# Kernel optimization log

Hardware: AMD Instinct MI355X
Metric: run time of the kernel (lower is better)

## Reference

```python
import jax, jax.numpy as jnp
import numpy as np

B = 65536          # bs * m
N_NODES = 2        # fixed by module usage (job-machine pair graphs)
IN_FEAT = 256
N_HEADS = 4
N_HIDDEN = 256     # concat=False -> n_hidden = out_features
SLOPE = 0.2


def setup_inputs() -> dict:
    key = jax.random.key(0)
    k_h, k_adj, k_w, k_a = jax.random.split(key, 4)
    h = jax.random.normal(k_h, (B, N_NODES, IN_FEAT), dtype=jnp.float32)
    # adjacency: ij=1 means edge j->i; force self-loops on the diagonal
    adj = jax.random.randint(k_adj, (B, 1, N_NODES, N_NODES), 0, 2, dtype=jnp.int32)
    diag = jnp.arange(N_NODES)
    adj = adj.at[..., diag, diag].set(1)
    # xavier-normal-ish scales
    W = jax.random.normal(k_w, (IN_FEAT, N_HIDDEN * N_HEADS), dtype=jnp.float32) * (2.0 / (IN_FEAT + N_HIDDEN * N_HEADS)) ** 0.5
    a = jax.random.normal(k_a, (N_HEADS, 2 * N_HIDDEN, 1), dtype=jnp.float32) * (2.0 / (2 * N_HIDDEN + 1)) ** 0.5
    return {"h": h, "adj_mat": adj, "W": W, "a": a}


def reference(h, adj_mat, W, a):
    # h: (B, N, F_in); W: (F_in, H*D); a: (H, 2D, 1); adj_mat: (B, 1, N, N)
    Bsz, n_nodes, _ = h.shape
    n_heads = a.shape[0]
    n_hidden = a.shape[1] // 2
    # (B, N, H*D) -> (B, H, N, D)
    ht = (h @ W).reshape(Bsz, n_nodes, n_heads, n_hidden).transpose(0, 2, 1, 3)
    # attention scores: e[b,h,i,j] = leakyrelu(src[b,h,i] + tgt[b,h,j])
    src = jnp.einsum('bhnd,hd->bhn', ht, a[:, :n_hidden, 0])
    tgt = jnp.einsum('bhnd,hd->bhn', ht, a[:, n_hidden:, 0])
    e = jax.nn.leaky_relu(src[..., :, None] + tgt[..., None, :], SLOPE)
    e = jnp.where(adj_mat > 0, e, -jnp.inf)  # (B, H, N, N)
    attn = jax.nn.softmax(e, axis=-1)
    h_prime = jnp.einsum('bhij,bhjd->bhid', attn, ht)  # (B, H, N, D)
    # concat=False -> mean over heads
    return h_prime.mean(axis=1)  # (B, N, D)
```

## Files before the change

### kernel.cpp

```cpp
#include <hip/hip_runtime.h>
#include <hip/hip_bf16.h>


typedef __attribute__((ext_vector_type(8))) short short8;
typedef __attribute__((ext_vector_type(4))) float floatx4;

__device__ __forceinline__ float bf2f(short u) {
    union { unsigned int i; float f; } v;
    v.i = ((unsigned int)(unsigned short)u) << 16;
    return v.f;
}
__device__ __forceinline__ unsigned int f2bf(float f) {
    union { float fv; unsigned int i; } v;
    v.fv = f;
    return (v.i + 0x7fffu + ((v.i >> 16) & 1u)) >> 16;
}

__global__ void prep_p(const float* __restrict__ W,
                       const float* __restrict__ a,
                       __hip_bfloat16* __restrict__ PT) {
    int tid = blockIdx.x * 256 + threadIdx.x;
    int h = tid >> 8, k = tid & 255;
    const float4* wrow = (const float4*)(W + k * 1024 + h * 256);
    const float4* a1 = (const float4*)(a + h * 512);
    const float4* a2 = (const float4*)(a + h * 512 + 256);
    float p1 = 0.f, p2 = 0.f;
    #pragma unroll 4
    for (int s = 0; s < 64; ++s) {
        float4 wv = wrow[s], v1 = a1[s], v2 = a2[s];
        p1 += wv.x * v1.x + wv.y * v1.y + wv.z * v1.z + wv.w * v1.w;
        p2 += wv.x * v2.x + wv.y * v2.y + wv.z * v2.z + wv.w * v2.w;
    }
    PT[h * 256 + k] = __float2bfloat16(p1);
    PT[(4 + h) * 256 + k] = __float2bfloat16(p2);
    PT[(8 + h) * 256 + k] = __float2bfloat16(0.f);
    PT[(12 + h) * 256 + k] = __float2bfloat16(0.f);
}

__global__ void prep_wt(const float* __restrict__ W,
                        __hip_bfloat16* __restrict__ Wt) {
    int idx = blockIdx.x * 256 + threadIdx.x;
    int d = idx >> 10, kk = idx & 1023;
    int h = kk >> 8, k = kk & 255;
    Wt[idx] = __float2bfloat16(W[k * 1024 + h * 256 + d]);
}

#define TB 64
#define ROWS 128
#define HS 264
#define WCH 72

__global__ __launch_bounds__(256, 1)
void gat_main(const float* __restrict__ hin,
              const int* __restrict__ adj,
              const __hip_bfloat16* __restrict__ PT,
              const __hip_bfloat16* __restrict__ Wt,
              float* __restrict__ out) {
    __shared__ __align__(16) __hip_bfloat16 sH[ROWS][HS];
    __shared__ __align__(16) __hip_bfloat16 sW[256][WCH];
    __shared__ __align__(16) __hip_bfloat16 sZ[ROWS][WCH];
    __shared__ __align__(16) __hip_bfloat16 sPT[16][HS];
    __shared__ __align__(16) float sS[ROWS][16];
    __shared__ __align__(16) float2 sC[TB * 4 * 2];

    const int tid = threadIdx.x;
    const int lane = tid & 63;
    const int wave = tid >> 6;
    const int m = lane & 15;
    const int q = lane >> 4;
    const long batch0 = (long)blockIdx.x * TB;

    #pragma unroll
    for (int it = 0; it < 2; ++it) {
        int idx = tid + it * 256;
        int n = idx >> 5, cg = idx & 31;
        int4 v = ((const int4*)PT)[idx];
        *(int4*)&sPT[n][cg * 8] = v;
    }
    {
        const float4* gh = (const float4*)(hin + batch0 * 512);
        #pragma unroll
        for (int it = 0; it < 32; ++it) {
            int idx = tid + it * 256;
            int r = idx >> 6, c4 = idx & 63;
            float4 v = gh[idx];
            ushort4 b;
            b.x = (unsigned short)f2bf(v.x);
            b.y = (unsigned short)f2bf(v.y);
            b.z = (unsigned short)f2bf(v.z);
            b.w = (unsigned short)f2bf(v.w);
            *(ushort4*)&sH[r][c4 * 4] = b;
        }
    }
    __syncthreads();

    {
        floatx4 a0 = {0.f, 0.f, 0.f, 0.f}, a1 = {0.f, 0.f, 0.f, 0.f};
        #pragma unroll
        for (int ks = 0; ks < 8; ++ks) {
            short8 bf = *(const short8*)&sPT[m][ks * 32 + q * 8];
            short8 f0 = *(const short8*)&sH[wave * 32 + m][ks * 32 + q * 8];
            short8 f1 = *(const short8*)&sH[wave * 32 + 16 + m][ks * 32 + q * 8];
            a0 = __builtin_amdgcn_mfma_f32_16x16x32_bf16(f0, bf, a0, 0, 0, 0);
            a1 = __builtin_amdgcn_mfma_f32_16x16x32_bf16(f1, bf, a1, 0, 0, 0);
        }
        #pragma unroll
        for (int r = 0; r < 4; ++r) {
            sS[wave * 32 + q * 4 + r][m] = a0[r];
            sS[wave * 32 + 16 + q * 4 + r][m] = a1[r];
        }
    }
    __syncthreads();

    {
        int lb = tid >> 2, hh = tid & 3;
        int4 av = ((const int4*)adj)[batch0 + lb];
        float s0 = sS[lb * 2][hh],     s1 = sS[lb * 2 + 1][hh];
        float t0 = sS[lb * 2][4 + hh], t1 = sS[lb * 2 + 1][4 + hh];
        float e00 = s0 + t0; e00 = e00 >= 0.f ? e00 : 0.2f * e00;
        float e01 = s0 + t1; e01 = e01 >= 0.f ? e01 : 0.2f * e01;
        float e10 = s1 + t0; e10 = e10 >= 0.f ? e10 : 0.2f * e10;
        float e11 = s1 + t1; e11 = e11 >= 0.f ? e11 : 0.2f * e11;
        e00 = fminf(fmaxf(e00, -80.f), 80.f);
        e01 = fminf(fmaxf(e01, -80.f), 80.f);
        e10 = fminf(fmaxf(e10, -80.f), 80.f);
        e11 = fminf(fmaxf(e11, -80.f), 80.f);
        {
            bool k0 = av.x > 0, k1 = av.y > 0;
            float f0 = k0 ? e00 : -1e30f, f1 = k1 ? e01 : -1e30f;
            float mx = fmaxf(f0, f1);
            float p0 = k0 ? __expf(e00 - mx) : 0.f;
            float p1 = k1 ? __expf(e01 - mx) : 0.f;
            float den = p0 + p1;
            float inv = den > 1e-30f ? 0.25f / den : 0.f;
            sC[(lb * 4 + hh) * 2 + 0] = make_float2(p0 * inv, p1 * inv);
        }
        {
            bool k0 = av.z > 0, k1 = av.w > 0;
            float f0 = k0 ? e10 : -1e30f, f1 = k1 ? e11 : -1e30f;
            float mx = fmaxf(f0, f1);
            float p0 = k0 ? __expf(e10 - mx) : 0.f;
            float p1 = k1 ? __expf(e11 - mx) : 0.f;
            float den = p0 + p1;
            float inv = den > 1e-30f ? 0.25f / den : 0.f;
            sC[(lb * 4 + hh) * 2 + 1] = make_float2(p0 * inv, p1 * inv);
        }
    }

    floatx4 acc[8][4];
    #pragma unroll
    for (int i = 0; i < 8; ++i)
        #pragma unroll
        for (int j = 0; j < 4; ++j)
            acc[i][j] = (floatx4){0.f, 0.f, 0.f, 0.f};

    #pragma unroll 1
    for (int hh = 0; hh < 4; ++hh) {
        #pragma unroll 1
        for (int kc = 0; kc < 4; ++kc) {
            __syncthreads();
            {
                const __hip_bfloat16* wg = Wt + hh * 256 + kc * 64;
                int cg = tid & 7, dbase = tid >> 3;
                #pragma unroll
                for (int it = 0; it < 8; ++it) {
                    int d = dbase + it * 32;
                    int4 v = *(const int4*)(wg + (long)d * 1024 + cg * 8);
                    *(int4*)&sW[d][cg * 8] = v;
                }
            }
            {
                int g = tid & 7, rbase = tid >> 3;
                #pragma unroll
                for (int it = 0; it < 4; ++it) {
                    int zr = rbase + it * 32;
                    float2 c = sC[((zr >> 1) * 4 + hh) * 2 + (zr & 1)];
                    int hr = zr & ~1;
                    short8 v0 = *(const short8*)&sH[hr][kc * 64 + g * 8];
                    short8 v1 = *(const short8*)&sH[hr + 1][kc * 64 + g * 8];
                    int4 zv; int* zp = (int*)&zv;
                    #pragma unroll
                    for (int jj = 0; jj < 4; ++jj) {
                        float z0 = c.x * bf2f(v0[jj * 2])     + c.y * bf2f(v1[jj * 2]);
                        float z1 = c.x * bf2f(v0[jj * 2 + 1]) + c.y * bf2f(v1[jj * 2 + 1]);
                        zp[jj] = (int)(f2bf(z0) | (f2bf(z1) << 16));
                    }
                    *(int4*)&sZ[zr][g * 8] = zv;
                }
            }
            __syncthreads();
            #pragma unroll
            for (int ks = 0; ks < 2; ++ks) {
                short8 bfr[4];
                #pragma unroll
                for (int nt = 0; nt < 4; ++nt)
                    bfr[nt] = *(const short8*)&sW[wave * 64 + nt * 16 + m][ks * 32 + q * 8];
                #pragma unroll
                for (int mt = 0; mt < 8; ++mt) {
                    short8 af = *(const short8*)&sZ[mt * 16 + m][ks * 32 + q * 8];
                    #pragma unroll
                    for (int nt = 0; nt < 4; ++nt)
                        acc[mt][nt] = __builtin_amdgcn_mfma_f32_16x16x32_bf16(
                            af, bfr[nt], acc[mt][nt], 0, 0, 0);
                }
            }
        }
    }

    {
        float* og = out + batch0 * 512;
        #pragma unroll
        for (int mt = 0; mt < 8; ++mt)
            #pragma unroll
            for (int nt = 0; nt < 4; ++nt) {
                int col = wave * 64 + nt * 16 + m;
                #pragma unroll
                for (int r = 0; r < 4; ++r)
                    og[(mt * 16 + q * 4 + r) * 256 + col] = acc[mt][nt][r];
            }
    }
}

extern "C" void kernel_launch(void* const* d_in, const int* in_sizes, int n_in,
                              void* d_out, int out_size, void* d_ws, size_t ws_size,
                              hipStream_t stream) {
    const float* hin = (const float*)d_in[0];
    const int* adj   = (const int*)d_in[1];
    const float* W   = (const float*)d_in[2];
    const float* a   = (const float*)d_in[3];
    float* out       = (float*)d_out;

    __hip_bfloat16* PT = (__hip_bfloat16*)d_ws;
    __hip_bfloat16* Wt = PT + 16 * 256;

    if (ws_size < (16 * 256 + 256 * 1024) * sizeof(__hip_bfloat16)) return;

    int B = in_sizes[0] / 512;
    prep_p<<<4, 256, 0, stream>>>(W, a, PT);
    prep_wt<<<(256 * 1024) / 256, 256, 0, stream>>>(W, Wt);
    gat_main<<<B / TB, 256, 0, stream>>>(hin, adj, PT, Wt, out);
}
```

Before: 361.1 us.

## Halve batch tile, load W fragments directly from global, raise occupancy

Halves the per-block batch tile to 32 (64 rows) and stops staging W through shared memory. W is pre-swizzled into an MFMA-fragment-friendly layout (Wt2) and each wave reads its B fragments directly from global/L2. The freed LDS, plus aliasing the score buffers onto the Z buffer, lets launch bounds allow 3 blocks per CU for better latency hiding. The two prep kernels are merged into one using wave-reduction dot products, and conversions use packed bf16 intrinsics. The trade-off is that W is now re-read from cache for every block instead of once per block tile.

```diff
diff --git a/kernel.cpp b/kernel.cpp
--- a/kernel.cpp
+++ b/kernel.cpp
@@ -10,58 +10,53 @@
     v.i = ((unsigned int)(unsigned short)u) << 16;
     return v.f;
 }
-__device__ __forceinline__ unsigned int f2bf(float f) {
-    union { float fv; unsigned int i; } v;
-    v.fv = f;
-    return (v.i + 0x7fffu + ((v.i >> 16) & 1u)) >> 16;
-}
-
-__global__ void prep_p(const float* __restrict__ W,
-                       const float* __restrict__ a,
-                       __hip_bfloat16* __restrict__ PT) {
-    int tid = blockIdx.x * 256 + threadIdx.x;
-    int h = tid >> 8, k = tid & 255;
-    const float4* wrow = (const float4*)(W + k * 1024 + h * 256);
-    const float4* a1 = (const float4*)(a + h * 512);
-    const float4* a2 = (const float4*)(a + h * 512 + 256);
-    float p1 = 0.f, p2 = 0.f;
-    #pragma unroll 4
-    for (int s = 0; s < 64; ++s) {
-        float4 wv = wrow[s], v1 = a1[s], v2 = a2[s];
-        p1 += wv.x * v1.x + wv.y * v1.y + wv.z * v1.z + wv.w * v1.w;
-        p2 += wv.x * v2.x + wv.y * v2.y + wv.z * v2.z + wv.w * v2.w;
-    }
-    PT[h * 256 + k] = __float2bfloat16(p1);
-    PT[(4 + h) * 256 + k] = __float2bfloat16(p2);
-    PT[(8 + h) * 256 + k] = __float2bfloat16(0.f);
-    PT[(12 + h) * 256 + k] = __float2bfloat16(0.f);
-}
-
-__global__ void prep_wt(const float* __restrict__ W,
-                        __hip_bfloat16* __restrict__ Wt) {
-    int idx = blockIdx.x * 256 + threadIdx.x;
-    int d = idx >> 10, kk = idx & 1023;
-    int h = kk >> 8, k = kk & 255;
-    Wt[idx] = __float2bfloat16(W[k * 1024 + h * 256 + d]);
-}
-
-#define TB 64
-#define ROWS 128
+__device__ __forceinline__ unsigned int pk2(float lo, float hi) {
+    __hip_bfloat162 t = __float22bfloat162_rn(make_float2(lo, hi));
+    union { __hip_bfloat162 h; unsigned int u; } cv; cv.h = t;
+    return cv.u;
+}
+
+__global__ void gat_prep(const float* __restrict__ W, const float* __restrict__ a,
+                         __hip_bfloat16* __restrict__ PT,
+                         __hip_bfloat16* __restrict__ Wt2) {
+    int b = blockIdx.x;
+    if (b < 1024) {
+        int idx = b * 256 + threadIdx.x;
+        int d = idx & 255, hh = (idx >> 8) & 3, k = idx >> 10;
+        int j = k >> 5, kl = k & 31;
+        Wt2[(((hh * 8 + j) * 256 + d) << 5) + kl] =
+            __float2bfloat16(W[k * 1024 + hh * 256 + d]);
+    } else {
+        int wid = (b - 1024) * 4 + (threadIdx.x >> 6);
+        int lane = threadIdx.x & 63;
+        int k = wid & 255, h = (wid >> 8) & 3, half = wid >> 10;
+        float4 wv = *(const float4*)(W + k * 1024 + h * 256 + lane * 4);
+        float4 av = *(const float4*)(a + h * 512 + half * 256 + lane * 4);
+        float s = wv.x * av.x + wv.y * av.y + wv.z * av.z + wv.w * av.w;
+        #pragma unroll
+        for (int off = 32; off; off >>= 1) s += __shfl_down(s, off);
+        if (lane == 0) PT[(half * 4 + h) * 256 + k] = __float2bfloat16(s);
+        if (lane == 1) PT[2048 + wid] = __float2bfloat16(0.f);
+    }
+}
+
+#define TB 32
+#define ROWS 64
 #define HS 264
-#define WCH 72
-
-__global__ __launch_bounds__(256, 1)
+#define ZS 136
+
+__global__ __launch_bounds__(256, 3)
 void gat_main(const float* __restrict__ hin,
               const int* __restrict__ adj,
               const __hip_bfloat16* __restrict__ PT,
-              const __hip_bfloat16* __restrict__ Wt,
+              const __hip_bfloat16* __restrict__ Wt2,
               float* __restrict__ out) {
     __shared__ __align__(16) __hip_bfloat16 sH[ROWS][HS];
-    __shared__ __align__(16) __hip_bfloat16 sW[256][WCH];
-    __shared__ __align__(16) __hip_bfloat16 sZ[ROWS][WCH];
-    __shared__ __align__(16) __hip_bfloat16 sPT[16][HS];
-    __shared__ __align__(16) float sS[ROWS][16];
+    __shared__ __align__(16) unsigned char uZ[ROWS * ZS * 2];
     __shared__ __align__(16) float2 sC[TB * 4 * 2];
+    __hip_bfloat16 (*sZ)[ZS]  = (__hip_bfloat16 (*)[ZS])uZ;
+    __hip_bfloat16 (*sPT)[HS] = (__hip_bfloat16 (*)[HS])uZ;
+    float (*sS)[16] = (float (*)[16])(uZ + 8448);
 
     const int tid = threadIdx.x;
     const int lane = tid & 63;
@@ -80,76 +75,55 @@
     {
         const float4* gh = (const float4*)(hin + batch0 * 512);
         #pragma unroll
-        for (int it = 0; it < 32; ++it) {
+        for (int it = 0; it < 16; ++it) {
             int idx = tid + it * 256;
             int r = idx >> 6, c4 = idx & 63;
             float4 v = gh[idx];
-            ushort4 b;
-            b.x = (unsigned short)f2bf(v.x);
-            b.y = (unsigned short)f2bf(v.y);
-            b.z = (unsigned short)f2bf(v.z);
-            b.w = (unsigned short)f2bf(v.w);
-            *(ushort4*)&sH[r][c4 * 4] = b;
+            uint2 bv;
+            bv.x = pk2(v.x, v.y);
+            bv.y = pk2(v.z, v.w);
+            *(uint2*)&sH[r][c4 * 4] = bv;
         }
     }
     __syncthreads();
 
     {
-        floatx4 a0 = {0.f, 0.f, 0.f, 0.f}, a1 = {0.f, 0.f, 0.f, 0.f};
+        floatx4 a0 = {0.f, 0.f, 0.f, 0.f};
         #pragma unroll
         for (int ks = 0; ks < 8; ++ks) {
             short8 bf = *(const short8*)&sPT[m][ks * 32 + q * 8];
-            short8 f0 = *(const short8*)&sH[wave * 32 + m][ks * 32 + q * 8];
-            short8 f1 = *(const short8*)&sH[wave * 32 + 16 + m][ks * 32 + q * 8];
+            short8 f0 = *(const short8*)&sH[wave * 16 + m][ks * 32 + q * 8];
             a0 = __builtin_amdgcn_mfma_f32_16x16x32_bf16(f0, bf, a0, 0, 0, 0);
-            a1 = __builtin_amdgcn_mfma_f32_16x16x32_bf16(f1, bf, a1, 0, 0, 0);
         }
         #pragma unroll
-        for (int r = 0; r < 4; ++r) {
-            sS[wave * 32 + q * 4 + r][m] = a0[r];
-            sS[wave * 32 + 16 + q * 4 + r][m] = a1[r];
-        }
+        for (int r = 0; r < 4; ++r)
+            sS[wave * 16 + q * 4 + r][m] = a0[r];
     }
     __syncthreads();
 
     {
-        int lb = tid >> 2, hh = tid & 3;
+        int lb = tid >> 3, hh = (tid >> 1) & 3, i = tid & 1;
         int4 av = ((const int4*)adj)[batch0 + lb];
-        float s0 = sS[lb * 2][hh],     s1 = sS[lb * 2 + 1][hh];
+        int m0 = i ? av.z : av.x, m1 = i ? av.w : av.y;
+        float s  = sS[lb * 2 + i][hh];
         float t0 = sS[lb * 2][4 + hh], t1 = sS[lb * 2 + 1][4 + hh];
-        float e00 = s0 + t0; e00 = e00 >= 0.f ? e00 : 0.2f * e00;
-        float e01 = s0 + t1; e01 = e01 >= 0.f ? e01 : 0.2f * e01;
-        float e10 = s1 + t0; e10 = e10 >= 0.f ? e10 : 0.2f * e10;
-        float e11 = s1 + t1; e11 = e11 >= 0.f ? e11 : 0.2f * e11;
-        e00 = fminf(fmaxf(e00, -80.f), 80.f);
-        e01 = fminf(fmaxf(e01, -80.f), 80.f);
-        e10 = fminf(fmaxf(e10, -80.f), 80.f);
-        e11 = fminf(fmaxf(e11, -80.f), 80.f);
-        {
-            bool k0 = av.x > 0, k1 = av.y > 0;
-            float f0 = k0 ? e00 : -1e30f, f1 = k1 ? e01 : -1e30f;
-            float mx = fmaxf(f0, f1);
-            float p0 = k0 ? __expf(e00 - mx) : 0.f;
-            float p1 = k1 ? __expf(e01 - mx) : 0.f;
-            float den = p0 + p1;
-            float inv = den > 1e-30f ? 0.25f / den : 0.f;
-            sC[(lb * 4 + hh) * 2 + 0] = make_float2(p0 * inv, p1 * inv);
-        }
-        {
-            bool k0 = av.z > 0, k1 = av.w > 0;
-            float f0 = k0 ? e10 : -1e30f, f1 = k1 ? e11 : -1e30f;
-            float mx = fmaxf(f0, f1);
-            float p0 = k0 ? __expf(e10 - mx) : 0.f;
-            float p1 = k1 ? __expf(e11 - mx) : 0.f;
-            float den = p0 + p1;
-            float inv = den > 1e-30f ? 0.25f / den : 0.f;
-            sC[(lb * 4 + hh) * 2 + 1] = make_float2(p0 * inv, p1 * inv);
-        }
-    }
-
-    floatx4 acc[8][4];
+        float e0 = s + t0; e0 = e0 >= 0.f ? e0 : 0.2f * e0;
+        float e1 = s + t1; e1 = e1 >= 0.f ? e1 : 0.2f * e1;
+        e0 = fminf(fmaxf(e0, -80.f), 80.f);
+        e1 = fminf(fmaxf(e1, -80.f), 80.f);
+        bool k0 = m0 > 0, k1 = m1 > 0;
+        float f0 = k0 ? e0 : -1e30f, f1 = k1 ? e1 : -1e30f;
+        float mx = fmaxf(f0, f1);
+        float p0 = k0 ? __expf(e0 - mx) : 0.f;
+        float p1 = k1 ? __expf(e1 - mx) : 0.f;
+        float den = p0 + p1;
+        float inv = den > 1e-30f ? 0.25f / den : 0.f;
+        sC[(lb * 4 + hh) * 2 + i] = make_float2(p0 * inv, p1 * inv);
+    }
+
+    floatx4 acc[4][4];
     #pragma unroll
-    for (int i = 0; i < 8; ++i)
+    for (int i = 0; i < 4; ++i)
         #pragma unroll
         for (int j = 0; j < 4; ++j)
             acc[i][j] = (floatx4){0.f, 0.f, 0.f, 0.f};
@@ -157,47 +131,40 @@
     #pragma unroll 1
     for (int hh = 0; hh < 4; ++hh) {
         #pragma unroll 1
-        for (int kc = 0; kc < 4; ++kc) {
+        for (int s = 0; s < 2; ++s) {
             __syncthreads();
             {
-                const __hip_bfloat16* wg = Wt + hh * 256 + kc * 64;
-                int cg = tid & 7, dbase = tid >> 3;
-                #pragma unroll
-                for (int it = 0; it < 8; ++it) {
-                    int d = dbase + it * 32;
-                    int4 v = *(const int4*)(wg + (long)d * 1024 + cg * 8);
-                    *(int4*)&sW[d][cg * 8] = v;
-                }
-            }
-            {
-                int g = tid & 7, rbase = tid >> 3;
+                int g = tid & 15, rb = tid >> 4;
                 #pragma unroll
                 for (int it = 0; it < 4; ++it) {
-                    int zr = rbase + it * 32;
+                    int zr = rb + it * 16;
                     float2 c = sC[((zr >> 1) * 4 + hh) * 2 + (zr & 1)];
                     int hr = zr & ~1;
-                    short8 v0 = *(const short8*)&sH[hr][kc * 64 + g * 8];
-                    short8 v1 = *(const short8*)&sH[hr + 1][kc * 64 + g * 8];
+                    short8 v0 = *(const short8*)&sH[hr][s * 128 + g * 8];
+                    short8 v1 = *(const short8*)&sH[hr + 1][s * 128 + g * 8];
                     int4 zv; int* zp = (int*)&zv;
                     #pragma unroll
                     for (int jj = 0; jj < 4; ++jj) {
                         float z0 = c.x * bf2f(v0[jj * 2])     + c.y * bf2f(v1[jj * 2]);
                         float z1 = c.x * bf2f(v0[jj * 2 + 1]) + c.y * bf2f(v1[jj * 2 + 1]);
-                        zp[jj] = (int)(f2bf(z0) | (f2bf(z1) << 16));
+                        zp[jj] = (int)pk2(z0, z1);
                     }
                     *(int4*)&sZ[zr][g * 8] = zv;
                 }
             }
             __syncthreads();
             #pragma unroll
-            for (int ks = 0; ks < 2; ++ks) {
+            for (int js = 0; js < 4; ++js) {
+                int jg = hh * 8 + s * 4 + js;
+                const short* wb = (const short*)Wt2 +
+                                  ((jg * 256 + wave * 64 + m) << 5) + q * 8;
                 short8 bfr[4];
                 #pragma unroll
                 for (int nt = 0; nt < 4; ++nt)
-                    bfr[nt] = *(const short8*)&sW[wave * 64 + nt * 16 + m][ks * 32 + q * 8];
-                #pragma unroll
-                for (int mt = 0; mt < 8; ++mt) {
-                    short8 af = *(const short8*)&sZ[mt * 16 + m][ks * 32 + q * 8];
+                    bfr[nt] = *(const short8*)(wb + nt * 512);
+                #pragma unroll
+                for (int mt = 0; mt < 4; ++mt) {
+                    short8 af = *(const short8*)&sZ[mt * 16 + m][js * 32 + q * 8];
                     #pragma unroll
                     for (int nt = 0; nt < 4; ++nt)
                         acc[mt][nt] = __builtin_amdgcn_mfma_f32_16x16x32_bf16(
@@ -210,7 +177,7 @@
     {
         float* og = out + batch0 * 512;
         #pragma unroll
-        for (int mt = 0; mt < 8; ++mt)
+        for (int mt = 0; mt < 4; ++mt)
             #pragma unroll
             for (int nt = 0; nt < 4; ++nt) {
                 int col = wave * 64 + nt * 16 + m;
@@ -230,13 +197,12 @@
     const float* a   = (const float*)d_in[3];
     float* out       = (float*)d_out;
 
-    __hip_bfloat16* PT = (__hip_bfloat16*)d_ws;
-    __hip_bfloat16* Wt = PT + 16 * 256;
+    __hip_bfloat16* PT  = (__hip_bfloat16*)d_ws;
+    __hip_bfloat16* Wt2 = PT + 16 * 256;
 
     if (ws_size < (16 * 256 + 256 * 1024) * sizeof(__hip_bfloat16)) return;
 
     int B = in_sizes[0] / 512;
-    prep_p<<<4, 256, 0, stream>>>(W, a, PT);
-    prep_wt<<<(256 * 1024) / 256, 256, 0, stream>>>(W, Wt);
-    gat_main<<<B / TB, 256, 0, stream>>>(hin, adj, PT, Wt, out);
-}
+    gat_prep<<<1536, 256, 0, stream>>>(W, a, PT, Wt2);
+    gat_main<<<B / TB, 256, 0, stream>>>(hin, adj, PT, Wt2, out);
+}
```

Result: faster. 293.4 us (-18.7%).
